# Performance work log

Hardware: AMD Instinct MI355X
Metric: run time of the kernel (lower is better)

## Reference

```python
import jax, jax.numpy as jnp
import numpy as np

N = 50000       # nodes
E = 1600000     # edges (avg degree 32)
D = 128         # h_dim
R = 20          # num_rels = 2 * n_labels
L = 2           # RelGraphConv layers (2*n_layers // 2)


def setup_inputs() -> dict:
    key = jax.random.key(0)
    ks = jax.random.split(key, 7)
    node_embeddings = jax.random.normal(ks[0], (N, D), dtype=jnp.float32)
    edge_src = jax.random.randint(ks[1], (E,), 0, N, dtype=jnp.int32)
    edge_dst = jax.random.randint(ks[2], (E,), 0, N, dtype=jnp.int32)
    etypes = jax.random.randint(ks[3], (E,), 0, R, dtype=jnp.int32)
    # per-layer learned params (DGL RelGraphConv, regularizer=None):
    # W: per-relation weight [L, R, D, D]; loop_w: self-loop weight; bias.
    W = jax.random.normal(ks[4], (L, R, D, D), dtype=jnp.float32) / np.float32(np.sqrt(D))
    loop_w = jax.random.normal(ks[5], (L, D, D), dtype=jnp.float32) / np.float32(np.sqrt(D))
    bias = jax.random.normal(ks[6], (L, D), dtype=jnp.float32) * 0.01
    return {
        "node_embeddings": node_embeddings,
        "W": W,
        "loop_w": loop_w,
        "bias": bias,
        "edge_src": edge_src,
        "edge_dst": edge_dst,
        "etypes": etypes,
    }


def reference(node_embeddings, W, loop_w, bias, edge_src, edge_dst, etypes):
    # Stacked RelGraphConv: msg_e = h[src_e] @ W[rel_e]; sum-scatter to dst;
    # h' = agg + h @ loop_w + bias (no activation applied in module forward).
    h = node_embeddings
    num_nodes = h.shape[0]
    for l in range(L):
        # transform every node by every relation once: [N, R, D]
        hW = jnp.einsum('ni,rio->nro', h, W[l])
        msg = hW[edge_src, etypes]                                  # [E, D] gather
        agg = jax.ops.segment_sum(msg, edge_dst, num_segments=num_nodes)
        h = agg + h @ loop_w[l] + bias[l]
    return h
```

## Files before the change

kernel.cpp:

```cpp
#include <hip/hip_runtime.h>
#include <hip/hip_bf16.h>
#include <stdint.h>


#define NN 50000
#define NE 1600000
#define DIM 128
#define NREL 20
#define NRELP 21
#define TILE 16
#define NTILE (NN / TILE)
#define CELLS (NN * NREL)
#define CHB 200
#define CHE (NE / CHB)
#define TT_N (NTILE * CHB)
#define SCAN_EPB 2048
#define NBLK_TT ((TT_N + SCAN_EPB - 1) / SCAN_EPB)
#define SPK_CAP 1024
#define PACKED_ELEMS (2 * NRELP * 4 * 8 * 64 * 8)

typedef __attribute__((ext_vector_type(8))) short short8;
typedef __attribute__((ext_vector_type(4))) float f32x4;

__device__ __forceinline__ unsigned short f32_to_bf16_raw(float f) {
  union { float f; unsigned u; } c; c.f = f;
  unsigned u = c.u;
  return (unsigned short)((u + 0x7fffu + ((u >> 16) & 1u)) >> 16);
}
__device__ __forceinline__ unsigned cvt_pk_bf16(float lo, float hi) {
  unsigned r;
  asm("v_cvt_pk_bf16_f32 %0, %1, %2" : "=v"(r) : "v"(lo), "v"(hi));
  return r;
}

__global__ void cvt_bf16_kernel(const float* __restrict__ in,
                                unsigned short* __restrict__ out, int n4) {
  int i = blockIdx.x * 256 + threadIdx.x;
  if (i < n4) {
    float4 f = ((const float4*)in)[i];
    unsigned long long p =
        (unsigned long long)cvt_pk_bf16(f.x, f.y)
      | ((unsigned long long)cvt_pk_bf16(f.z, f.w) << 32);
    __builtin_nontemporal_store(p, (unsigned long long*)out + i);
  }
}

__global__ void pack_w_kernel(const float* __restrict__ W,
                              const float* __restrict__ loop_w,
                              unsigned short* __restrict__ WP) {
  int idx = blockIdx.x * 256 + threadIdx.x;
  if (idx >= PACKED_ELEMS) return;
  int j = idx & 7;       int t = idx >> 3;
  int lane = t & 63;     t >>= 6;
  int nc = t & 7;        t >>= 3;
  int ks = t & 3;        t >>= 2;
  int r = t % NRELP;     int l = t / NRELP;
  int k = ks * 32 + (lane >> 4) * 8 + j;
  int n = nc * 16 + (lane & 15);
  float v = (r < NREL) ? W[(((size_t)l * NREL + r) * DIM + k) * DIM + n]
                       : loop_w[((size_t)l * DIM + k) * DIM + n];
  WP[idx] = f32_to_bf16_raw(v);
}

__global__ __launch_bounds__(256) void tile_count_kernel(
    const int* __restrict__ dst, unsigned int* __restrict__ tt) {
  __shared__ unsigned int hist[NTILE];
  for (int i = threadIdx.x; i < NTILE; i += 256) hist[i] = 0u;
  __syncthreads();
  const int base = blockIdx.x * CHE;
  for (int i = base + threadIdx.x; i < base + CHE; i += 256)
    atomicAdd(&hist[dst[i] >> 4], 1u);
  __syncthreads();
  for (int i = threadIdx.x; i < NTILE; i += 256)
    tt[(size_t)i * CHB + blockIdx.x] = hist[i];
}

__global__ void scanA_kernel(const unsigned int* __restrict__ in,
                             unsigned int* __restrict__ out,
                             unsigned int* __restrict__ btot, int n) {
  __shared__ unsigned int buf[256];
  int tid = threadIdx.x;
  int base = blockIdx.x * SCAN_EPB + tid * 8;
  unsigned int v[8], p[8], s = 0;
#pragma unroll
  for (int j = 0; j < 8; ++j) {
    v[j] = (base + j < n) ? in[base + j] : 0u;
    p[j] = s; s += v[j];
  }
  buf[tid] = s;
  __syncthreads();
  for (int d = 1; d < 256; d <<= 1) {
    unsigned int a = (tid >= d) ? buf[tid - d] : 0u;
    __syncthreads();
    buf[tid] += a;
    __syncthreads();
  }
  unsigned int excl = buf[tid] - s;
#pragma unroll
  for (int j = 0; j < 8; ++j)
    if (base + j < n) out[base + j] = excl + p[j];
  if (tid == 255) btot[blockIdx.x] = buf[255];
}

__global__ void scanB_kernel(unsigned int* __restrict__ btot,
                             unsigned int* __restrict__ out, int nblk, int n) {
  __shared__ unsigned int buf[1024];
  int t = threadIdx.x;
  unsigned int v = (t < nblk) ? btot[t] : 0u;
  buf[t] = v;
  __syncthreads();
  for (int d = 1; d < 1024; d <<= 1) {
    unsigned int a = (t >= d) ? buf[t - d] : 0u;
    __syncthreads();
    buf[t] += a;
    __syncthreads();
  }
  if (t < nblk) btot[t] = buf[t] - v;
  if (t == 1023) out[n] = buf[1023];
}

__global__ void scanC_kernel(const unsigned int* __restrict__ btot,
                             unsigned int* __restrict__ out, int n) {
  int base = blockIdx.x * SCAN_EPB + threadIdx.x * 8;
  unsigned int add = btot[blockIdx.x];
#pragma unroll
  for (int j = 0; j < 8; ++j)
    if (base + j < n) out[base + j] += add;
}

__global__ __launch_bounds__(256) void tile_scatter_kernel(
    const int* __restrict__ src, const int* __restrict__ dst,
    const int* __restrict__ et, const unsigned int* __restrict__ tts,
    unsigned int* __restrict__ ep) {
  __shared__ unsigned int cur[NTILE];
  for (int i = threadIdx.x; i < NTILE; i += 256)
    cur[i] = tts[(size_t)i * CHB + blockIdx.x];
  __syncthreads();
  const int base = blockIdx.x * CHE;
  for (int i = base + threadIdx.x; i < base + CHE; i += 256) {
    int d = dst[i];
    unsigned int pos = atomicAdd(&cur[d >> 4], 1u);
    ep[pos] = (unsigned int)src[i] | ((unsigned int)(d & 15) << 16)
            | ((unsigned int)et[i] << 20);
  }
}

__global__ __launch_bounds__(512) void tile_sort_kernel(
    const unsigned int* __restrict__ ep, const unsigned int* __restrict__ tts,
    unsigned short* __restrict__ es, unsigned int* __restrict__ cofs) {
  __shared__ unsigned int hist[512];
  const int t = threadIdx.x;
  const int tile = blockIdx.x;
  const unsigned int start = tts[(size_t)tile * CHB];
  const unsigned int end = (tile + 1 < NTILE) ? tts[(size_t)(tile + 1) * CHB]
                                              : (unsigned int)NE;
  const int cnt = (int)(end - start);
  hist[t] = 0u;
  __syncthreads();
  for (int i = t; i < cnt; i += 512) {
    unsigned int p = ep[start + i];
    atomicAdd(&hist[((p >> 16) & 15u) * 20u + (p >> 20)], 1u);
  }
  __syncthreads();
  unsigned int own = hist[t];
  for (int d = 1; d < 512; d <<= 1) {
    __syncthreads();
    unsigned int a = (t >= d) ? hist[t - d] : 0u;
    __syncthreads();
    hist[t] += a;
  }
  __syncthreads();
  unsigned int excl = hist[t] - own;
  hist[t] = excl;
  if (t < 320) cofs[(size_t)tile * 320 + t] = start + excl;
  if (tile == NTILE - 1 && t == 0) cofs[CELLS] = (unsigned int)NE;
  __syncthreads();
  for (int i = t; i < cnt; i += 512) {
    unsigned int p = ep[start + i];
    int sub = (int)(((p >> 16) & 15u) * 20u + (p >> 20));
    unsigned int rk = atomicAdd(&hist[sub], 1u);
    es[start + rk] = (unsigned short)(p & 0xffffu);
  }
}

__global__ __launch_bounds__(512, 8) void rgcn_layer_kernel(
    const unsigned short* __restrict__ hb,
    const unsigned short* __restrict__ WP,
    const float* __restrict__ bias,
    int layer,
    const unsigned int* __restrict__ cofs,
    const unsigned short* __restrict__ es,
    float* __restrict__ outf,
    unsigned short* __restrict__ outb)
{
  __shared__ short8 Sb8[TILE * 80];
  __shared__ unsigned int cofs_l[321];
  __shared__ unsigned short spk[SPK_CAP];

  const int tid  = threadIdx.x;
  const int lane = tid & 63;
  const int w    = tid >> 6;
  const int quad = lane >> 4;
  const int m    = lane & 15;
  const int mh8  = m * 8;
  const int half = w >> 2;
  const int g    = (w & 3) * 4 + quad;
  const int dst_base = blockIdx.x * TILE;

  for (int i = tid; i < 321; i += 512) cofs_l[i] = cofs[blockIdx.x * (TILE * NREL) + i];
  __syncthreads();
  const int e0 = (int)cofs_l[0];
  const int etot = (int)cofs_l[320] - e0;
  for (int i = tid; i < etot && i < SPK_CAP; i += 512) spk[i] = es[e0 + i];
  __syncthreads();

  f32x4 acc = (f32x4){0.f, 0.f, 0.f, 0.f};

  for (int c = 0; c < 5; ++c) {
    if (c < 4) {
      const int cbase = g * NREL + c * 5;
      const int rlA = half ? 2 : 0;
      const int rlB = half ? 5 : 2;
      const int beg    = (int)cofs_l[cbase + rlA] - e0;
      const int endAll = (int)cofs_l[cbase + rlB] - e0;

      float a0 = 0.f, a1 = 0.f, a2 = 0.f, a3 = 0.f;
      float a4 = 0.f, a5 = 0.f, a6 = 0.f, a7 = 0.f;
      int rl = rlA;
      int nend = (int)cofs_l[cbase + rl + 1] - e0;

      auto flush = [&]() {
        union { uint4 u; short8 s; } pk;
        pk.u.x = cvt_pk_bf16(a0, a1);
        pk.u.y = cvt_pk_bf16(a2, a3);
        pk.u.z = cvt_pk_bf16(a4, a5);
        pk.u.w = cvt_pk_bf16(a6, a7);
        Sb8[g * 80 + ((rl * 16 + m) ^ g)] = pk.s;
        a0 = a1 = a2 = a3 = a4 = a5 = a6 = a7 = 0.f;
      };
      auto bump = [&](int i) {
        while (i >= nend) {
          flush();
          ++rl;
          nend = (int)cofs_l[cbase + rl + 1] - e0;
        }
      };
      auto add8 = [&](short8 hv) {
        union { short8 s; uint4 u; } cv; cv.s = hv;
        a0 += __uint_as_float(cv.u.x << 16);
        a1 += __uint_as_float(cv.u.x & 0xffff0000u);
        a2 += __uint_as_float(cv.u.y << 16);
        a3 += __uint_as_float(cv.u.y & 0xffff0000u);
        a4 += __uint_as_float(cv.u.z << 16);
        a5 += __uint_as_float(cv.u.z & 0xffff0000u);
        a6 += __uint_as_float(cv.u.w << 16);
        a7 += __uint_as_float(cv.u.w & 0xffff0000u);
      };
      auto run_walk = [&](auto fetch) {
        for (int i = beg; i < endAll; i += 4) {
          const int nrem = endAll - i;
          short8 h0, h1, h2, h3;
          h0 = fetch(i);
          if (nrem > 1) h1 = fetch(i + 1);
          if (nrem > 2) h2 = fetch(i + 2);
          if (nrem > 3) h3 = fetch(i + 3);
          bump(i);      add8(h0);
          if (nrem > 1) { bump(i + 1); add8(h1); }
          if (nrem > 2) { bump(i + 2); add8(h2); }
          if (nrem > 3) { bump(i + 3); add8(h3); }
        }
        while (rl < rlB) { flush(); ++rl; }
      };

      if (endAll <= SPK_CAP) {
        run_walk([&](int i) {
          return *(const short8*)(hb + (size_t)spk[i] * DIM + mh8);
        });
      } else {
        run_walk([&](int i) {
          return *(const short8*)(hb + (size_t)es[e0 + i] * DIM + mh8);
        });
      }
    } else if (half == 0) {
      short8 hv = *(const short8*)(hb + (size_t)(dst_base + g) * DIM + mh8);
      Sb8[g * 80 + (m ^ g)] = hv;
    }
    __syncthreads();

    const int rc = (c == 4) ? 1 : 5;
    for (int rl2 = 0; rl2 < rc; ++rl2) {
      const int r = (c == 4) ? (NRELP - 1) : (c * 5 + rl2);
      const unsigned short* bp =
          WP + ((((size_t)(layer * NRELP + r) * 4) * 8 + w) * 64 + lane) * 8;
#pragma unroll
      for (int ks = 0; ks < 4; ++ks) {
        short8 a = Sb8[m * 80 + ((rl2 * 16 + ks * 4 + quad) ^ m)];
        short8 b = *(const short8*)(bp + (size_t)ks * 4096);
        acc = __builtin_amdgcn_mfma_f32_16x16x32_bf16(a, b, acc, 0, 0, 0);
      }
    }
    __syncthreads();
  }

  const int col = w * 16 + m;
  const float bv = bias[col];
  if (outb) {
#pragma unroll
    for (int i = 0; i < 4; ++i)
      outb[(size_t)(dst_base + quad * 4 + i) * DIM + col] =
          f32_to_bf16_raw(acc[i] + bv);
  } else {
#pragma unroll
    for (int i = 0; i < 4; ++i)
      outf[(size_t)(dst_base + quad * 4 + i) * DIM + col] = acc[i] + bv;
  }
}

extern "C" void kernel_launch(void* const* d_in, const int* in_sizes, int n_in,
                              void* d_out, int out_size, void* d_ws, size_t ws_size,
                              hipStream_t stream) {
  const float* h0     = (const float*)d_in[0];
  const float* W      = (const float*)d_in[1];
  const float* loop_w = (const float*)d_in[2];
  const float* bias   = (const float*)d_in[3];
  const int* esrc     = (const int*)d_in[4];
  const int* edst     = (const int*)d_in[5];
  const int* etyp     = (const int*)d_in[6];
  float* out = (float*)d_out;

  char* ws = (char*)d_ws;
  size_t off = 0;
  auto alloc = [&](size_t bytes) -> void* {
    void* p = ws + off;
    off = (off + bytes + 255) & ~(size_t)255;
    return p;
  };
  unsigned short* hb0   = (unsigned short*)alloc((size_t)NN * DIM * 2);
  unsigned short* hb1   = (unsigned short*)alloc((size_t)NN * DIM * 2);
  unsigned short* WP    = (unsigned short*)alloc((size_t)PACKED_ELEMS * 2);
  unsigned int*   tt    = (unsigned int*)alloc((size_t)(TT_N + 1) * 4);
  unsigned int*   tts   = (unsigned int*)alloc((size_t)(TT_N + 1) * 4);
  unsigned int*   btot  = (unsigned int*)alloc((size_t)NBLK_TT * 4);
  unsigned int*   ep    = (unsigned int*)alloc((size_t)NE * 4);
  unsigned int*   cofs  = (unsigned int*)alloc((size_t)(CELLS + 1) * 4);
  unsigned short* es    = (unsigned short*)alloc((size_t)NE * 2);

  tile_count_kernel<<<CHB, 256, 0, stream>>>(edst, tt);
  scanA_kernel<<<NBLK_TT, 256, 0, stream>>>(tt, tts, btot, TT_N);
  scanB_kernel<<<1, 1024, 0, stream>>>(btot, tts, NBLK_TT, TT_N);
  scanC_kernel<<<NBLK_TT, 256, 0, stream>>>(btot, tts, TT_N);
  tile_scatter_kernel<<<CHB, 256, 0, stream>>>(esrc, edst, etyp, tts, ep);
  tile_sort_kernel<<<NTILE, 512, 0, stream>>>(ep, tts, es, cofs);

  pack_w_kernel<<<(PACKED_ELEMS + 255) / 256, 256, 0, stream>>>(W, loop_w, WP);
  cvt_bf16_kernel<<<(NN * DIM / 4 + 255) / 256, 256, 0, stream>>>(h0, hb0, NN * DIM / 4);

  rgcn_layer_kernel<<<NTILE, 512, 0, stream>>>(hb0, WP, bias, 0, cofs, es,
                                               nullptr, hb1);
  rgcn_layer_kernel<<<NTILE, 512, 0, stream>>>(hb1, WP, bias + DIM, 1, cofs, es,
                                               out, nullptr);
}
```

Measured before the change: 404.8 us.

## Aggregate edge messages via one-hot MFMA instead of scalar per-lane accumulation

Result: slower. 509.2 us (+25.8%).

```diff
diff --git a/kernel.cpp b/kernel.cpp
--- a/kernel.cpp
+++ b/kernel.cpp
@@ -10,13 +10,12 @@
 #define NRELP 21
 #define TILE 16
 #define NTILE (NN / TILE)
-#define CELLS (NN * NREL)
 #define CHB 200
 #define CHE (NE / CHB)
 #define TT_N (NTILE * CHB)
 #define SCAN_EPB 2048
 #define NBLK_TT ((TT_N + SCAN_EPB - 1) / SCAN_EPB)
-#define SPK_CAP 1024
+#define ESP_CAP 640
 #define PACKED_ELEMS (2 * NRELP * 4 * 8 * 64 * 8)
 
 typedef __attribute__((ext_vector_type(8))) short short8;
@@ -55,7 +54,8 @@
   int nc = t & 7;        t >>= 3;
   int ks = t & 3;        t >>= 2;
   int r = t % NRELP;     int l = t / NRELP;
-  int k = ks * 32 + (lane >> 4) * 8 + j;
+  int kq = lane >> 4;
+  int k = ks * 32 + ((j < 4) ? (kq * 4 + j) : (16 + kq * 4 + (j - 4)));
   int n = nc * 16 + (lane & 15);
   float v = (r < NREL) ? W[(((size_t)l * NREL + r) * DIM + k) * DIM + n]
                        : loop_w[((size_t)l * DIM + k) * DIM + n];
@@ -102,8 +102,7 @@
   if (tid == 255) btot[blockIdx.x] = buf[255];
 }
 
-__global__ void scanB_kernel(unsigned int* __restrict__ btot,
-                             unsigned int* __restrict__ out, int nblk, int n) {
+__global__ void scanB_kernel(unsigned int* __restrict__ btot, int nblk) {
   __shared__ unsigned int buf[1024];
   int t = threadIdx.x;
   unsigned int v = (t < nblk) ? btot[t] : 0u;
@@ -116,7 +115,6 @@
     __syncthreads();
   }
   if (t < nblk) btot[t] = buf[t] - v;
-  if (t == 1023) out[n] = buf[1023];
 }
 
 __global__ void scanC_kernel(const unsigned int* __restrict__ btot,
@@ -147,39 +145,34 @@
 
 __global__ __launch_bounds__(512) void tile_sort_kernel(
     const unsigned int* __restrict__ ep, const unsigned int* __restrict__ tts,
-    unsigned short* __restrict__ es, unsigned int* __restrict__ cofs) {
-  __shared__ unsigned int hist[512];
+    unsigned int* __restrict__ esp, unsigned int* __restrict__ relofs) {
+  __shared__ unsigned int hist[NREL];
+  __shared__ unsigned int cur[NREL];
   const int t = threadIdx.x;
   const int tile = blockIdx.x;
   const unsigned int start = tts[(size_t)tile * CHB];
   const unsigned int end = (tile + 1 < NTILE) ? tts[(size_t)(tile + 1) * CHB]
                                               : (unsigned int)NE;
   const int cnt = (int)(end - start);
-  hist[t] = 0u;
+  if (t < NREL) hist[t] = 0u;
+  __syncthreads();
+  for (int i = t; i < cnt; i += 512)
+    atomicAdd(&hist[ep[start + i] >> 20], 1u);
+  __syncthreads();
+  if (t == 0) {
+    unsigned int run = start;
+    for (int r = 0; r < NREL; ++r) {
+      relofs[(size_t)tile * NRELP + r] = run;
+      cur[r] = run;
+      run += hist[r];
+    }
+    relofs[(size_t)tile * NRELP + NREL] = end;
+  }
   __syncthreads();
   for (int i = t; i < cnt; i += 512) {
     unsigned int p = ep[start + i];
-    atomicAdd(&hist[((p >> 16) & 15u) * 20u + (p >> 20)], 1u);
-  }
-  __syncthreads();
-  unsigned int own = hist[t];
-  for (int d = 1; d < 512; d <<= 1) {
-    __syncthreads();
-    unsigned int a = (t >= d) ? hist[t - d] : 0u;
-    __syncthreads();
-    hist[t] += a;
-  }
-  __syncthreads();
-  unsigned int excl = hist[t] - own;
-  hist[t] = excl;
-  if (t < 320) cofs[(size_t)tile * 320 + t] = start + excl;
-  if (tile == NTILE - 1 && t == 0) cofs[CELLS] = (unsigned int)NE;
-  __syncthreads();
-  for (int i = t; i < cnt; i += 512) {
-    unsigned int p = ep[start + i];
-    int sub = (int)(((p >> 16) & 15u) * 20u + (p >> 20));
-    unsigned int rk = atomicAdd(&hist[sub], 1u);
-    es[start + rk] = (unsigned short)(p & 0xffffu);
+    unsigned int pos = atomicAdd(&cur[p >> 20], 1u);
+    esp[pos] = p & 0xFFFFFu;
   }
 }
 
@@ -188,131 +181,145 @@
     const unsigned short* __restrict__ WP,
     const float* __restrict__ bias,
     int layer,
-    const unsigned int* __restrict__ cofs,
-    const unsigned short* __restrict__ es,
+    const unsigned int* __restrict__ relofs,
+    const unsigned int* __restrict__ esp,
     float* __restrict__ outf,
     unsigned short* __restrict__ outb)
 {
-  __shared__ short8 Sb8[TILE * 80];
-  __shared__ unsigned int cofs_l[321];
-  __shared__ unsigned short spk[SPK_CAP];
+  __shared__ __align__(16) unsigned short Hs[2][4096];
+  __shared__ __align__(16) unsigned short SbT[2048];
+  __shared__ unsigned int esp_l[ESP_CAP];
+  __shared__ unsigned short dl[2][32];
+  __shared__ unsigned int ro_l[NRELP];
 
   const int tid  = threadIdx.x;
   const int lane = tid & 63;
   const int w    = tid >> 6;
-  const int quad = lane >> 4;
-  const int m    = lane & 15;
-  const int mh8  = m * 8;
-  const int half = w >> 2;
-  const int g    = (w & 3) * 4 + quad;
+  const int q    = lane >> 4;
+  const int mm   = lane & 15;
   const int dst_base = blockIdx.x * TILE;
 
-  for (int i = tid; i < 321; i += 512) cofs_l[i] = cofs[blockIdx.x * (TILE * NREL) + i];
-  __syncthreads();
-  const int e0 = (int)cofs_l[0];
-  const int etot = (int)cofs_l[320] - e0;
-  for (int i = tid; i < etot && i < SPK_CAP; i += 512) spk[i] = es[e0 + i];
-  __syncthreads();
-
-  f32x4 acc = (f32x4){0.f, 0.f, 0.f, 0.f};
-
-  for (int c = 0; c < 5; ++c) {
-    if (c < 4) {
-      const int cbase = g * NREL + c * 5;
-      const int rlA = half ? 2 : 0;
-      const int rlB = half ? 5 : 2;
-      const int beg    = (int)cofs_l[cbase + rlA] - e0;
-      const int endAll = (int)cofs_l[cbase + rlB] - e0;
-
-      float a0 = 0.f, a1 = 0.f, a2 = 0.f, a3 = 0.f;
-      float a4 = 0.f, a5 = 0.f, a6 = 0.f, a7 = 0.f;
-      int rl = rlA;
-      int nend = (int)cofs_l[cbase + rl + 1] - e0;
-
-      auto flush = [&]() {
-        union { uint4 u; short8 s; } pk;
-        pk.u.x = cvt_pk_bf16(a0, a1);
-        pk.u.y = cvt_pk_bf16(a2, a3);
-        pk.u.z = cvt_pk_bf16(a4, a5);
-        pk.u.w = cvt_pk_bf16(a6, a7);
-        Sb8[g * 80 + ((rl * 16 + m) ^ g)] = pk.s;
-        a0 = a1 = a2 = a3 = a4 = a5 = a6 = a7 = 0.f;
-      };
-      auto bump = [&](int i) {
-        while (i >= nend) {
-          flush();
-          ++rl;
-          nend = (int)cofs_l[cbase + rl + 1] - e0;
-        }
-      };
-      auto add8 = [&](short8 hv) {
-        union { short8 s; uint4 u; } cv; cv.s = hv;
-        a0 += __uint_as_float(cv.u.x << 16);
-        a1 += __uint_as_float(cv.u.x & 0xffff0000u);
-        a2 += __uint_as_float(cv.u.y << 16);
-        a3 += __uint_as_float(cv.u.y & 0xffff0000u);
-        a4 += __uint_as_float(cv.u.z << 16);
-        a5 += __uint_as_float(cv.u.z & 0xffff0000u);
-        a6 += __uint_as_float(cv.u.w << 16);
-        a7 += __uint_as_float(cv.u.w & 0xffff0000u);
-      };
-      auto run_walk = [&](auto fetch) {
-        for (int i = beg; i < endAll; i += 4) {
-          const int nrem = endAll - i;
-          short8 h0, h1, h2, h3;
-          h0 = fetch(i);
-          if (nrem > 1) h1 = fetch(i + 1);
-          if (nrem > 2) h2 = fetch(i + 2);
-          if (nrem > 3) h3 = fetch(i + 3);
-          bump(i);      add8(h0);
-          if (nrem > 1) { bump(i + 1); add8(h1); }
-          if (nrem > 2) { bump(i + 2); add8(h2); }
-          if (nrem > 3) { bump(i + 3); add8(h3); }
-        }
-        while (rl < rlB) { flush(); ++rl; }
-      };
-
-      if (endAll <= SPK_CAP) {
-        run_walk([&](int i) {
-          return *(const short8*)(hb + (size_t)spk[i] * DIM + mh8);
-        });
-      } else {
-        run_walk([&](int i) {
-          return *(const short8*)(hb + (size_t)es[e0 + i] * DIM + mh8);
-        });
+  if (tid < NRELP) ro_l[tid] = relofs[(size_t)blockIdx.x * NRELP + tid];
+  __syncthreads();
+  const int e0 = (int)ro_l[0];
+  const int etot = (int)ro_l[NREL] - e0;
+  const bool use_lds = (etot <= ESP_CAP);
+  if (use_lds)
+    for (int i = tid; i < etot; i += 512) esp_l[i] = esp[e0 + i];
+  __syncthreads();
+
+  const unsigned hs_base  = (unsigned)(size_t)&Hs[0][0];
+  const unsigned sbt_base = (unsigned)(size_t)&SbT[0];
+
+  const int se = tid >> 4;
+  const int sm = tid & 15;
+
+  auto cntr = [&](int r) -> int {
+    return (r < NREL) ? (int)(ro_l[r + 1] - ro_l[r]) : 16;
+  };
+  auto next_re = [&](int r, int b) {
+    int nb = (cntr(r) + 31) >> 5;
+    if (r == NREL) nb = 1;
+    if (b + 1 < nb) return r * 32 + (b + 1);
+    int rn = r + 1;
+    while (rn < NREL && cntr(rn) == 0) ++rn;
+    if (rn > NREL) return -1;
+    return rn * 32;
+  };
+
+  short8 pv; int pd;
+  auto issue_load = [&](int r, int b) {
+    int src, dL;
+    if (r < NREL) {
+      int ge = (int)ro_l[r] + b * 32 + se;
+      bool pad = ge >= (int)ro_l[r + 1];
+      int gi = pad ? ((int)ro_l[r + 1] - 1) : ge;
+      unsigned p = use_lds ? esp_l[gi - e0] : esp[gi];
+      src = (int)(p & 0xFFFFu);
+      dL = pad ? 31 : (int)((p >> 16) & 15u);
+    } else {
+      bool pad = se >= 16;
+      src = dst_base + (pad ? 15 : se);
+      dL = pad ? 31 : se;
+    }
+    pd = dL;
+    pv = *(const short8*)(hb + (size_t)src * DIM + sm * 8);
+  };
+
+  f32x4 accS = (f32x4){0.f, 0.f, 0.f, 0.f};
+  f32x4 accO = (f32x4){0.f, 0.f, 0.f, 0.f};
+
+  int rs = 0;
+  while (rs < NREL && cntr(rs) == 0) ++rs;
+  int bs = 0;
+  issue_load(rs, bs);
+  int buf = 0;
+
+  while (true) {
+    if (sm == 0) dl[buf][se] = (unsigned short)pd;
+    *(short8*)&Hs[buf][(sm >> 1) * 512 + se * 16 + (sm & 1) * 8] = pv;
+
+    const int nxt = next_re(rs, bs);
+    if (nxt >= 0) issue_load(nxt >> 5, nxt & 31);
+    __syncthreads();
+
+    short8 A;
+#pragma unroll
+    for (int j = 0; j < 8; ++j) {
+      int e = (j < 4) ? (q * 4 + j) : (16 + q * 4 + (j - 4));
+      A[j] = (dl[buf][e] == mm) ? (short)0x3F80 : (short)0;
+    }
+    {
+      unsigned ad = hs_base + (unsigned)buf * 8192u + (unsigned)w * 1024u
+                  + (unsigned)lane * 8u;
+      unsigned long long t0, t1;
+      asm volatile("ds_read_b64_tr_b16 %0, %1" : "=v"(t0) : "v"(ad) : "memory");
+      asm volatile("ds_read_b64_tr_b16 %0, %1" : "=v"(t1) : "v"(ad + 512u) : "memory");
+      asm volatile("s_waitcnt lgkmcnt(0)" ::: "memory");
+      __builtin_amdgcn_sched_barrier(0);
+      union { struct { unsigned long long a, b; } u; short8 s; } pk;
+      pk.u.a = t0; pk.u.b = t1;
+      accS = __builtin_amdgcn_mfma_f32_16x16x32_bf16(A, pk.s, accS, 0, 0, 0);
+    }
+
+    const bool rel_done = (nxt < 0) || ((nxt >> 5) != rs);
+    if (rel_done) {
+      unsigned p0 = cvt_pk_bf16(accS[0], accS[1]);
+      unsigned p1 = cvt_pk_bf16(accS[2], accS[3]);
+      *(uint2*)&SbT[w * 256 + mm * 16 + q * 4] = make_uint2(p0, p1);
+      accS = (f32x4){0.f, 0.f, 0.f, 0.f};
+      __syncthreads();
+      const unsigned short* bp =
+          WP + ((((size_t)(layer * NRELP + rs) * 4) * 8 + w) * 64 + lane) * 8;
+#pragma unroll
+      for (int ks = 0; ks < 4; ++ks) {
+        unsigned ad = sbt_base + (unsigned)ks * 1024u + (unsigned)lane * 8u;
+        unsigned long long t0, t1;
+        asm volatile("ds_read_b64_tr_b16 %0, %1" : "=v"(t0) : "v"(ad) : "memory");
+        asm volatile("ds_read_b64_tr_b16 %0, %1" : "=v"(t1) : "v"(ad + 512u) : "memory");
+        short8 B = *(const short8*)(bp + (size_t)ks * 4096);
+        asm volatile("s_waitcnt lgkmcnt(0)" ::: "memory");
+        __builtin_amdgcn_sched_barrier(0);
+        union { struct { unsigned long long a, b; } u; short8 s; } pk;
+        pk.u.a = t0; pk.u.b = t1;
+        accO = __builtin_amdgcn_mfma_f32_16x16x32_bf16(pk.s, B, accO, 0, 0, 0);
       }
-    } else if (half == 0) {
-      short8 hv = *(const short8*)(hb + (size_t)(dst_base + g) * DIM + mh8);
-      Sb8[g * 80 + (m ^ g)] = hv;
-    }
-    __syncthreads();
-
-    const int rc = (c == 4) ? 1 : 5;
-    for (int rl2 = 0; rl2 < rc; ++rl2) {
-      const int r = (c == 4) ? (NRELP - 1) : (c * 5 + rl2);
-      const unsigned short* bp =
-          WP + ((((size_t)(layer * NRELP + r) * 4) * 8 + w) * 64 + lane) * 8;
-#pragma unroll
-      for (int ks = 0; ks < 4; ++ks) {
-        short8 a = Sb8[m * 80 + ((rl2 * 16 + ks * 4 + quad) ^ m)];
-        short8 b = *(const short8*)(bp + (size_t)ks * 4096);
-        acc = __builtin_amdgcn_mfma_f32_16x16x32_bf16(a, b, acc, 0, 0, 0);
-      }
-    }
-    __syncthreads();
-  }
-
-  const int col = w * 16 + m;
+    }
+    if (nxt < 0) break;
+    rs = nxt >> 5; bs = nxt & 31; buf ^= 1;
+  }
+
+  const int col = w * 16 + mm;
   const float bv = bias[col];
   if (outb) {
 #pragma unroll
     for (int i = 0; i < 4; ++i)
-      outb[(size_t)(dst_base + quad * 4 + i) * DIM + col] =
-          f32_to_bf16_raw(acc[i] + bv);
+      outb[(size_t)(dst_base + q * 4 + i) * DIM + col] =
+          f32_to_bf16_raw(accO[i] + bv);
   } else {
 #pragma unroll
     for (int i = 0; i < 4; ++i)
-      outf[(size_t)(dst_base + quad * 4 + i) * DIM + col] = acc[i] + bv;
+      outf[(size_t)(dst_base + q * 4 + i) * DIM + col] = accO[i] + bv;
   }
 }
 
@@ -342,21 +349,21 @@
   unsigned int*   tts   = (unsigned int*)alloc((size_t)(TT_N + 1) * 4);
   unsigned int*   btot  = (unsigned int*)alloc((size_t)NBLK_TT * 4);
   unsigned int*   ep    = (unsigned int*)alloc((size_t)NE * 4);
-  unsigned int*   cofs  = (unsigned int*)alloc((size_t)(CELLS + 1) * 4);
-  unsigned short* es    = (unsigned short*)alloc((size_t)NE * 2);
+  unsigned int*   esp   = (unsigned int*)alloc((size_t)NE * 4);
+  unsigned int*   relofs= (unsigned int*)alloc((size_t)(NTILE * NRELP + 1) * 4);
 
   tile_count_kernel<<<CHB, 256, 0, stream>>>(edst, tt);
   scanA_kernel<<<NBLK_TT, 256, 0, stream>>>(tt, tts, btot, TT_N);
-  scanB_kernel<<<1, 1024, 0, stream>>>(btot, tts, NBLK_TT, TT_N);
+  scanB_kernel<<<1, 1024, 0, stream>>>(btot, NBLK_TT);
   scanC_kernel<<<NBLK_TT, 256, 0, stream>>>(btot, tts, TT_N);
   tile_scatter_kernel<<<CHB, 256, 0, stream>>>(esrc, edst, etyp, tts, ep);
-  tile_sort_kernel<<<NTILE, 512, 0, stream>>>(ep, tts, es, cofs);
+  tile_sort_kernel<<<NTILE, 512, 0, stream>>>(ep, tts, esp, relofs);
 
   pack_w_kernel<<<(PACKED_ELEMS + 255) / 256, 256, 0, stream>>>(W, loop_w, WP);
   cvt_bf16_kernel<<<(NN * DIM / 4 + 255) / 256, 256, 0, stream>>>(h0, hb0, NN * DIM / 4);
 
-  rgcn_layer_kernel<<<NTILE, 512, 0, stream>>>(hb0, WP, bias, 0, cofs, es,
+  rgcn_layer_kernel<<<NTILE, 512, 0, stream>>>(hb0, WP, bias, 0, relofs, esp,
                                                nullptr, hb1);
-  rgcn_layer_kernel<<<NTILE, 512, 0, stream>>>(hb1, WP, bias + DIM, 1, cofs, es,
+  rgcn_layer_kernel<<<NTILE, 512, 0, stream>>>(hb1, WP, bias + DIM, 1, relofs, esp,
                                                out, nullptr);
 }
```

## Dynamically distribute (dst,relation) gather cells across wave quarters via LDS atomic counter

Applied to the files above, without the earlier changes.

Measured after the change: 418.9 us. 3.5% more time.

```diff
diff --git a/kernel.cpp b/kernel.cpp
--- a/kernel.cpp
+++ b/kernel.cpp
@@ -102,8 +102,7 @@
   if (tid == 255) btot[blockIdx.x] = buf[255];
 }
 
-__global__ void scanB_kernel(unsigned int* __restrict__ btot,
-                             unsigned int* __restrict__ out, int nblk, int n) {
+__global__ void scanB_kernel(unsigned int* __restrict__ btot, int nblk) {
   __shared__ unsigned int buf[1024];
   int t = threadIdx.x;
   unsigned int v = (t < nblk) ? btot[t] : 0u;
@@ -116,7 +115,6 @@
     __syncthreads();
   }
   if (t < nblk) btot[t] = buf[t] - v;
-  if (t == 1023) out[n] = buf[1023];
 }
 
 __global__ void scanC_kernel(const unsigned int* __restrict__ btot,
@@ -196,6 +194,7 @@
   __shared__ short8 Sb8[TILE * 80];
   __shared__ unsigned int cofs_l[321];
   __shared__ unsigned short spk[SPK_CAP];
+  __shared__ unsigned int ctr[4];
 
   const int tid  = threadIdx.x;
   const int lane = tid & 63;
@@ -203,85 +202,78 @@
   const int quad = lane >> 4;
   const int m    = lane & 15;
   const int mh8  = m * 8;
-  const int half = w >> 2;
   const int g    = (w & 3) * 4 + quad;
   const int dst_base = blockIdx.x * TILE;
 
   for (int i = tid; i < 321; i += 512) cofs_l[i] = cofs[blockIdx.x * (TILE * NREL) + i];
+  if (tid < 4) ctr[tid] = 0u;
   __syncthreads();
   const int e0 = (int)cofs_l[0];
   const int etot = (int)cofs_l[320] - e0;
-  for (int i = tid; i < etot && i < SPK_CAP; i += 512) spk[i] = es[e0 + i];
+  const bool use_lds = (etot <= SPK_CAP);
+  if (use_lds)
+    for (int i = tid; i < etot; i += 512) spk[i] = es[e0 + i];
   __syncthreads();
 
   f32x4 acc = (f32x4){0.f, 0.f, 0.f, 0.f};
 
   for (int c = 0; c < 5; ++c) {
     if (c < 4) {
-      const int cbase = g * NREL + c * 5;
-      const int rlA = half ? 2 : 0;
-      const int rlB = half ? 5 : 2;
-      const int beg    = (int)cofs_l[cbase + rlA] - e0;
-      const int endAll = (int)cofs_l[cbase + rlB] - e0;
-
-      float a0 = 0.f, a1 = 0.f, a2 = 0.f, a3 = 0.f;
-      float a4 = 0.f, a5 = 0.f, a6 = 0.f, a7 = 0.f;
-      int rl = rlA;
-      int nend = (int)cofs_l[cbase + rl + 1] - e0;
-
-      auto flush = [&]() {
+      for (;;) {
+        int k0 = 0;
+        if (m == 0) k0 = (int)atomicAdd(&ctr[c], 1u);
+        const int k = __shfl(k0, quad << 4);
+        if (k >= 80) break;
+        const int dd = k & 15;
+        const int rl = k >> 4;
+        const int idx = dd * NREL + c * 5 + rl;
+        const int beg = (int)cofs_l[idx] - e0;
+        const int end = (int)cofs_l[idx + 1] - e0;
+
+        float a0 = 0.f, a1 = 0.f, a2 = 0.f, a3 = 0.f;
+        float a4 = 0.f, a5 = 0.f, a6 = 0.f, a7 = 0.f;
+        auto add8 = [&](short8 hv) {
+          union { short8 s; uint4 u; } cv; cv.s = hv;
+          a0 += __uint_as_float(cv.u.x << 16);
+          a1 += __uint_as_float(cv.u.x & 0xffff0000u);
+          a2 += __uint_as_float(cv.u.y << 16);
+          a3 += __uint_as_float(cv.u.y & 0xffff0000u);
+          a4 += __uint_as_float(cv.u.z << 16);
+          a5 += __uint_as_float(cv.u.z & 0xffff0000u);
+          a6 += __uint_as_float(cv.u.w << 16);
+          a7 += __uint_as_float(cv.u.w & 0xffff0000u);
+        };
+        auto walk = [&](auto fetch) {
+          for (int i = beg; i < end; i += 4) {
+            const int nrem = end - i;
+            short8 h0, h1, h2, h3;
+            h0 = fetch(i);
+            if (nrem > 1) h1 = fetch(i + 1);
+            if (nrem > 2) h2 = fetch(i + 2);
+            if (nrem > 3) h3 = fetch(i + 3);
+            add8(h0);
+            if (nrem > 1) add8(h1);
+            if (nrem > 2) add8(h2);
+            if (nrem > 3) add8(h3);
+          }
+        };
+        if (use_lds) {
+          walk([&](int i) {
+            return *(const short8*)(hb + (size_t)spk[i] * DIM + mh8);
+          });
+        } else {
+          walk([&](int i) {
+            return *(const short8*)(hb + (size_t)es[e0 + i] * DIM + mh8);
+          });
+        }
         union { uint4 u; short8 s; } pk;
         pk.u.x = cvt_pk_bf16(a0, a1);
         pk.u.y = cvt_pk_bf16(a2, a3);
         pk.u.z = cvt_pk_bf16(a4, a5);
         pk.u.w = cvt_pk_bf16(a6, a7);
-        Sb8[g * 80 + ((rl * 16 + m) ^ g)] = pk.s;
-        a0 = a1 = a2 = a3 = a4 = a5 = a6 = a7 = 0.f;
-      };
-      auto bump = [&](int i) {
-        while (i >= nend) {
-          flush();
-          ++rl;
-          nend = (int)cofs_l[cbase + rl + 1] - e0;
-        }
-      };
-      auto add8 = [&](short8 hv) {
-        union { short8 s; uint4 u; } cv; cv.s = hv;
-        a0 += __uint_as_float(cv.u.x << 16);
-        a1 += __uint_as_float(cv.u.x & 0xffff0000u);
-        a2 += __uint_as_float(cv.u.y << 16);
-        a3 += __uint_as_float(cv.u.y & 0xffff0000u);
-        a4 += __uint_as_float(cv.u.z << 16);
-        a5 += __uint_as_float(cv.u.z & 0xffff0000u);
-        a6 += __uint_as_float(cv.u.w << 16);
-        a7 += __uint_as_float(cv.u.w & 0xffff0000u);
-      };
-      auto run_walk = [&](auto fetch) {
-        for (int i = beg; i < endAll; i += 4) {
-          const int nrem = endAll - i;
-          short8 h0, h1, h2, h3;
-          h0 = fetch(i);
-          if (nrem > 1) h1 = fetch(i + 1);
-          if (nrem > 2) h2 = fetch(i + 2);
-          if (nrem > 3) h3 = fetch(i + 3);
-          bump(i);      add8(h0);
-          if (nrem > 1) { bump(i + 1); add8(h1); }
-          if (nrem > 2) { bump(i + 2); add8(h2); }
-          if (nrem > 3) { bump(i + 3); add8(h3); }
-        }
-        while (rl < rlB) { flush(); ++rl; }
-      };
-
-      if (endAll <= SPK_CAP) {
-        run_walk([&](int i) {
-          return *(const short8*)(hb + (size_t)spk[i] * DIM + mh8);
-        });
-      } else {
-        run_walk([&](int i) {
-          return *(const short8*)(hb + (size_t)es[e0 + i] * DIM + mh8);
-        });
+        Sb8[dd * 80 + ((rl * 16 + m) ^ dd)] = pk.s;
       }
-    } else if (half == 0) {
+    } else if (w < 4) {
       short8 hv = *(const short8*)(hb + (size_t)(dst_base + g) * DIM + mh8);
       Sb8[g * 80 + (m ^ g)] = hv;
     }
@@ -347,7 +339,7 @@
 
   tile_count_kernel<<<CHB, 256, 0, stream>>>(edst, tt);
   scanA_kernel<<<NBLK_TT, 256, 0, stream>>>(tt, tts, btot, TT_N);
-  scanB_kernel<<<1, 1024, 0, stream>>>(btot, tts, NBLK_TT, TT_N);
+  scanB_kernel<<<1, 1024, 0, stream>>>(btot, NBLK_TT);
   scanC_kernel<<<NBLK_TT, 256, 0, stream>>>(btot, tts, TT_N);
   tile_scatter_kernel<<<CHB, 256, 0, stream>>>(esrc, edst, etyp, tts, ep);
   tile_sort_kernel<<<NTILE, 512, 0, stream>>>(ep, tts, es, cofs);
```
